# Performance work log

Measured on AMD Instinct MI355X. Metric: run time of the kernel, lower is better.

## Reference

```python
import jax, jax.numpy as jnp
import numpy as np

H = 16      # num_attention_heads
HKV = 4     # num_key_value_heads
HIDDEN = 1024
HEAD_DIM = HIDDEN // H  # 64
ROPE_BASE = 10000.0


def _rope(x):
    # Rotate-half RoPE applied over the FULL projected last dim, matching the
    # module which applies self._rope before splitting into heads.
    B, S, D = x.shape
    half = D // 2
    inv_freq = 1.0 / (ROPE_BASE ** (jnp.arange(half, dtype=jnp.float32) / half))
    ang = jnp.arange(S, dtype=jnp.float32)[:, None] * inv_freq[None, :]  # [S, half]
    cos, sin = jnp.cos(ang), jnp.sin(ang)
    x1, x2 = x[..., :half], x[..., half:]
    return jnp.concatenate([x1 * cos - x2 * sin, x2 * cos + x1 * sin], axis=-1)


def _rmsnorm(x):
    # F.rms_norm with no weight: x / sqrt(mean(x^2) + eps)
    eps = jnp.finfo(x.dtype).eps
    return x * jax.lax.rsqrt(jnp.mean(x * x, axis=-1, keepdims=True) + eps)


def setup_inputs() -> dict:
    key = jax.random.key(0)
    ks = jax.random.split(key, 10)
    B, S = 2, 2048
    kv_dim = HKV * HEAD_DIM
    sc = 0.02
    return {
        "hidden_state": jax.random.normal(ks[0], (B, S, HIDDEN), dtype=jnp.float32),
        "attention_mask": jnp.zeros((B, S, S), dtype=jnp.float32),
        "Wq": jax.random.normal(ks[1], (HIDDEN, HIDDEN), dtype=jnp.float32) * sc,
        "bq": jnp.zeros((HIDDEN,), dtype=jnp.float32),
        "Wk": jax.random.normal(ks[2], (HIDDEN, kv_dim), dtype=jnp.float32) * sc,
        "bk": jnp.zeros((kv_dim,), dtype=jnp.float32),
        "Wv": jax.random.normal(ks[3], (HIDDEN, kv_dim), dtype=jnp.float32) * sc,
        "bv": jnp.zeros((kv_dim,), dtype=jnp.float32),
        "Wo": jax.random.normal(ks[4], (HIDDEN, HIDDEN), dtype=jnp.float32) * sc,
        "bo": jnp.zeros((HIDDEN,), dtype=jnp.float32),
    }


def reference(hidden_state, attention_mask, Wq, bq, Wk, bk, Wv, bv, Wo, bo):
    B, S, _ = hidden_state.shape
    G = H // HKV  # query heads per kv head
    d = HEAD_DIM

    q = hidden_state @ Wq + bq            # [B,S,H*d]
    k = hidden_state @ Wk + bk            # [B,S,Hkv*d]
    v = hidden_state @ Wv + bv            # [B,S,Hkv*d]

    q = _rope(q)
    k = _rope(k)

    # split heads; repeat_interleave of KV over groups == grouping Q heads as [Hkv, G]
    q = q.reshape(B, S, H, d).transpose(0, 2, 1, 3).reshape(B, HKV, G, S, d)
    k = k.reshape(B, S, HKV, d).transpose(0, 2, 1, 3)   # [B,Hkv,S,d]
    v = v.reshape(B, S, HKV, d).transpose(0, 2, 1, 3)   # [B,Hkv,S,d]

    q = _rmsnorm(q)
    k = _rmsnorm(k)

    scale = d ** 0.5
    scores = jnp.einsum('bkgqd,bksd->bkgqs', q, k) / scale  # [B,Hkv,G,S,S]
    scores = scores + attention_mask[:, None, None, :, :]
    attn = jax.nn.softmax(scores, axis=-1)
    out = jnp.einsum('bkgqs,bksd->bkgqd', attn, v)          # [B,Hkv,G,S,d]

    out = out.reshape(B, H, S, d).transpose(0, 2, 1, 3).reshape(B, S, H * d)
    return out @ Wo + bo
```

## Files before the change

kernel.cpp:

```cpp
#include <hip/hip_runtime.h>
#include <cmath>

#define SEQ 2048
#define BATCH 2
#define HID 1024
#define NH 16
#define NKV 4
#define DH 64
#define KVDIM 256
#define K32C 32

typedef __attribute__((ext_vector_type(8))) short bf16x8;
typedef __attribute__((ext_vector_type(4))) float f32x4;

static __device__ __forceinline__ unsigned short f2bf(float x) {
  union { float f; unsigned u; } v; v.f = x;
  unsigned r = v.u + 0x7fffu + ((v.u >> 16) & 1u);
  return (unsigned short)(r >> 16);
}
static __device__ __forceinline__ float bf2f(unsigned short h) {
  union { unsigned u; float f; } v; v.u = ((unsigned)h) << 16;
  return v.f;
}
static __device__ __forceinline__ void gl_lds16(const void* g, void* l) {
  __builtin_amdgcn_global_load_lds(
      (const __attribute__((address_space(1))) unsigned int*)g,
      (__attribute__((address_space(3))) unsigned int*)l, 16, 0, 0);
}

template<bool HILO>
__global__ __launch_bounds__(256) void pack_a_kernel(
    const float* __restrict__ A, unsigned short* __restrict__ hi,
    unsigned short* __restrict__ lo) {
  int gid = blockIdx.x * 256 + threadIdx.x;
  int lane = gid & 63;
  int k32 = (gid >> 6) & 31;
  int m16 = gid >> 11;
  int quad = lane >> 4, l16 = lane & 15;
  const float* src = A + (size_t)(m16 * 16 + l16) * 1024 + k32 * 32 + quad * 8;
  float4 a0 = *(const float4*)src;
  float4 a1 = *(const float4*)(src + 4);
  float v[8] = {a0.x, a0.y, a0.z, a0.w, a1.x, a1.y, a1.z, a1.w};
  unsigned short h[8], l[8];
#pragma unroll
  for (int j = 0; j < 8; ++j) {
    h[j] = f2bf(v[j]);
    if (HILO) l[j] = f2bf(v[j] - bf2f(h[j]));
  }
  *(bf16x8*)(hi + (size_t)gid * 8) = *(bf16x8*)h;
  if (HILO) *(bf16x8*)(lo + (size_t)gid * 8) = *(bf16x8*)l;
}

__global__ __launch_bounds__(256) void pack_a_norm_kernel(
    const float* __restrict__ A, const float* __restrict__ lpart,
    unsigned short* __restrict__ hi, unsigned short* __restrict__ lo) {
  int gid = blockIdx.x * 256 + threadIdx.x;
  int lane = gid & 63;
  int k32 = (gid >> 6) & 31;
  int m16 = gid >> 11;
  int quad = lane >> 4, l16 = lane & 15;
  int m = m16 * 16 + l16;
  int b = m >> 11, s = m & 2047;
  int k0 = k32 * 32 + quad * 8;
  int h = k0 >> 6;
  float inv = 1.0f / lpart[(size_t)(b * NH + h) * SEQ + s];
  const float* src = A + (size_t)m * 1024 + k0;
  float4 a0 = *(const float4*)src;
  float4 a1 = *(const float4*)(src + 4);
  float v[8] = {a0.x, a0.y, a0.z, a0.w, a1.x, a1.y, a1.z, a1.w};
  unsigned short hh[8], ll[8];
#pragma unroll
  for (int j = 0; j < 8; ++j) {
    float x = v[j] * inv;
    hh[j] = f2bf(x);
    ll[j] = f2bf(x - bf2f(hh[j]));
  }
  *(bf16x8*)(hi + (size_t)gid * 8) = *(bf16x8*)hh;
  *(bf16x8*)(lo + (size_t)gid * 8) = *(bf16x8*)ll;
}

template<bool HILO>
__global__ __launch_bounds__(256) void pack_b_kernel(
    const float* __restrict__ W, unsigned short* __restrict__ hi,
    unsigned short* __restrict__ lo, int Nsrc) {
  int gid = blockIdx.x * 256 + threadIdx.x;
  int lane = gid & 63;
  int k32 = (gid >> 6) & 31;
  int n16 = gid >> 11;
  int quad = lane >> 4, l16 = lane & 15;
  int n = n16 * 16 + l16, k = k32 * 32 + quad * 8;
  unsigned short h[8], l[8];
#pragma unroll
  for (int j = 0; j < 8; ++j) {
    float v = W[(size_t)(k + j) * Nsrc + n];
    h[j] = f2bf(v);
    if (HILO) l[j] = f2bf(v - bf2f(h[j]));
  }
  *(bf16x8*)(hi + (size_t)gid * 8) = *(bf16x8*)h;
  if (HILO) *(bf16x8*)(lo + (size_t)gid * 8) = *(bf16x8*)l;
}

__global__ __launch_bounds__(256) void bias_cat_kernel(
    const float* __restrict__ bq, const float* __restrict__ bk,
    const float* __restrict__ bv, float* __restrict__ dst) {
  int n = blockIdx.x * 256 + threadIdx.x;
  if (n < 1536)
    dst[n] = (n < 1024) ? bq[n] : (n < 1280 ? bk[n - 1024] : bv[n - 1280]);
}

template<int CHAINS, bool OUTBF16>
__global__ __launch_bounds__(256) void gemm_pk_kernel(
    const unsigned short* __restrict__ Ah, const unsigned short* __restrict__ Al,
    const unsigned short* __restrict__ Bh, const unsigned short* __restrict__ Bl,
    const float* __restrict__ bias, void* __restrict__ Cout, int N) {
  constexpr int NCH = (CHAINS == 3) ? 2 : 1;
  __shared__ unsigned short Asm[NCH][4 * 512];
  __shared__ unsigned short Bsm[NCH][8 * 512];
  const int tid = threadIdx.x;
  const int wave = tid >> 6, lane = tid & 63;
  const int wr = wave >> 1, wc = wave & 1;
  const int quad = lane >> 4, l16 = lane & 15;
  const size_t abase = ((size_t)(blockIdx.y * 4 + wave) * K32C) * 64 + lane;
  const size_t bbase0 = ((size_t)(blockIdx.x * 8 + wave) * K32C) * 64 + lane;
  const size_t bbase1 = ((size_t)(blockIdx.x * 8 + wave + 4) * K32C) * 64 + lane;
  f32x4 acc[2][4] = {};
  for (int k32 = 0; k32 < K32C; ++k32) {
    __syncthreads();
    gl_lds16(Ah + (abase + (size_t)k32 * 64) * 8, &Asm[0][wave * 512]);
    gl_lds16(Bh + (bbase0 + (size_t)k32 * 64) * 8, &Bsm[0][wave * 512]);
    gl_lds16(Bh + (bbase1 + (size_t)k32 * 64) * 8, &Bsm[0][(wave + 4) * 512]);
    if (CHAINS == 3) {
      gl_lds16(Al + (abase + (size_t)k32 * 64) * 8, &Asm[1][wave * 512]);
      gl_lds16(Bl + (bbase0 + (size_t)k32 * 64) * 8, &Bsm[1][wave * 512]);
      gl_lds16(Bl + (bbase1 + (size_t)k32 * 64) * 8, &Bsm[1][(wave + 4) * 512]);
    }
    __syncthreads();
    bf16x8 af[2][NCH], bfr[4][NCH];
#pragma unroll
    for (int mt = 0; mt < 2; ++mt)
#pragma unroll
      for (int ch = 0; ch < NCH; ++ch)
        af[mt][ch] = *(const bf16x8*)&Asm[ch][((wr * 2 + mt) * 64 + lane) * 8];
#pragma unroll
    for (int nt = 0; nt < 4; ++nt)
#pragma unroll
      for (int ch = 0; ch < NCH; ++ch)
        bfr[nt][ch] = *(const bf16x8*)&Bsm[ch][((wc * 4 + nt) * 64 + lane) * 8];
#pragma unroll
    for (int mt = 0; mt < 2; ++mt)
#pragma unroll
      for (int nt = 0; nt < 4; ++nt) {
        acc[mt][nt] = __builtin_amdgcn_mfma_f32_16x16x32_bf16(af[mt][0], bfr[nt][0], acc[mt][nt], 0, 0, 0);
        if (CHAINS == 3) {
          acc[mt][nt] = __builtin_amdgcn_mfma_f32_16x16x32_bf16(af[mt][1], bfr[nt][0], acc[mt][nt], 0, 0, 0);
          acc[mt][nt] = __builtin_amdgcn_mfma_f32_16x16x32_bf16(af[mt][0], bfr[nt][1], acc[mt][nt], 0, 0, 0);
        }
      }
  }
  const int n0 = blockIdx.x * 128 + wc * 64;
  const int m0 = blockIdx.y * 64 + wr * 32;
#pragma unroll
  for (int mt = 0; mt < 2; ++mt)
#pragma unroll
    for (int nt = 0; nt < 4; ++nt)
#pragma unroll
      for (int r = 0; r < 4; ++r) {
        int gm = m0 + mt * 16 + quad * 4 + r;
        int n = n0 + nt * 16 + l16;
        float v = acc[mt][nt][r] + bias[n];
        if (OUTBF16)
          ((unsigned short*)Cout)[(size_t)gm * N + n] = f2bf(v);
        else
          ((float*)Cout)[(size_t)gm * N + n] = v;
      }
}

__global__ __launch_bounds__(1024) void rope_norm_q_kernel(
    const unsigned short* __restrict__ qkv, unsigned short* __restrict__ Qh,
    unsigned short* __restrict__ Ql) {
  const int s = blockIdx.x, b = blockIdx.y;
  const int t = threadIdx.x;
  const unsigned short* row = qkv + ((size_t)b * SEQ + s) * 1536;
  const int j = t & 511;
  float invf = exp2f((float)j * (-13.287712379549449f / 512.0f));
  float ang = (float)s * invf;
  float c = cosf(ang), sn = sinf(ang);
  float x1 = bf2f(row[j]), x2 = bf2f(row[j + 512]);
  float val = (t < 512) ? (x1 * c - x2 * sn) : (x2 * c + x1 * sn);
  float ss = val * val;
#pragma unroll
  for (int off = 1; off < 64; off <<= 1) ss += __shfl_xor(ss, off);
  float rn = rsqrtf(ss * (1.0f / 64.0f) + 1.1920929e-07f);
  float v = val * rn;
  unsigned short hi = f2bf(v);
  unsigned short lo = f2bf(v - bf2f(hi));
  int h = t >> 6, d = t & 63;
  size_t o = (size_t)(b * NH + h) * 131072 +
             ((((size_t)(s >> 4) * 2 + (d >> 5)) * 64) + ((d >> 3) & 3) * 16 + (s & 15)) * 8 + (d & 7);
  Qh[o] = hi;
  Ql[o] = lo;
}

__global__ __launch_bounds__(256) void rope_norm_kv_kernel(
    const unsigned short* __restrict__ qkv, unsigned short* __restrict__ Kpk,
    unsigned short* __restrict__ Vpk) {
  const int s = blockIdx.x, b = blockIdx.y;
  const int t = threadIdx.x;
  const unsigned short* row = qkv + ((size_t)b * SEQ + s) * 1536;
  const int j = t & 127;
  float invf = exp2f((float)j * (-13.287712379549449f / 128.0f));
  float ang = (float)s * invf;
  float c = cosf(ang), sn = sinf(ang);
  float x1 = bf2f(row[1024 + j]), x2 = bf2f(row[1024 + 128 + j]);
  float val = (t < 128) ? (x1 * c - x2 * sn) : (x2 * c + x1 * sn);
  float ss = val * val;
#pragma unroll
  for (int off = 1; off < 64; off <<= 1) ss += __shfl_xor(ss, off);
  float rn = rsqrtf(ss * (1.0f / 64.0f) + 1.1920929e-07f);
  float kv = val * rn;
  int h = t >> 6, d = t & 63;
  size_t ko = (size_t)(b * NKV + h) * 131072 +
              ((((size_t)(s >> 4) * 2 + (d >> 5)) * 64) + ((d >> 3) & 3) * 16 + (s & 15)) * 8 + (d & 7);
  Kpk[ko] = f2bf(kv);
  size_t vo = (size_t)(b * NKV + h) * 131072 +
              ((((size_t)(d >> 4) * 64 + (s >> 5)) * 64) + ((s >> 3) & 3) * 16 + (d & 15)) * 8 + (s & 7);
  Vpk[vo] = row[1280 + t];
}

__global__ __launch_bounds__(256, 4) void attn_mfma5_kernel(
    const unsigned short* __restrict__ Qh, const unsigned short* __restrict__ Ql,
    const unsigned short* __restrict__ Kpk, const unsigned short* __restrict__ Vpk,
    const float* __restrict__ mask, float* __restrict__ attn_po,
    float* __restrict__ l_part) {
  __shared__ __align__(16) unsigned short Kb[2][4 * 512];
  __shared__ __align__(16) unsigned short Vb[2][4 * 512];
  __shared__ __align__(16) float Msk[2][32 * 32];
  __shared__ __align__(16) unsigned short Ps[4][16 * 72];

  const int b = blockIdx.z;
  const int kvh = blockIdx.y >> 1, jh = blockIdx.y & 1;
  const int q0 = blockIdx.x * 32;
  const int tid = threadIdx.x, wave = tid >> 6, lane = tid & 63;
  const int quad = lane >> 4, l16 = lane & 15;
  const int h = kvh * 4 + wave;

  bf16x8 qh[2][2], ql[2][2];
  {
    const unsigned short* Qb_h = Qh + (size_t)(b * NH + h) * 131072;
    const unsigned short* Qb_l = Ql + (size_t)(b * NH + h) * 131072;
#pragma unroll
    for (int mt = 0; mt < 2; ++mt)
#pragma unroll
      for (int kf = 0; kf < 2; ++kf) {
        size_t o = ((((size_t)(q0 >> 4) + mt) * 2 + kf) * 64 + lane) * 8;
        qh[mt][kf] = *(const bf16x8*)(Qb_h + o);
        ql[mt][kf] = *(const bf16x8*)(Qb_l + o);
      }
  }

  const unsigned short* Kbase = Kpk + (size_t)(b * NKV + kvh) * 131072;
  const unsigned short* Vbase = Vpk + (size_t)(b * NKV + kvh) * 131072;
  const int jbase = jh * (SEQ / 2);

  const float* mbase = mask + ((size_t)b * SEQ + q0) * SEQ + jbase;
  const int srow = wave * 8 + (lane >> 3);
  const int ssw = ((srow >> 2) & 1) << 4;
  const float* msrc0 = mbase + (size_t)srow * SEQ + (((lane & 7) * 4) ^ ssw);

  bf16x8 ones;
#pragma unroll
  for (int i = 0; i < 8; ++i) ones[i] = (short)0x3F80;

  f32x4 O[2][4] = {};
  f32x4 lAcc[2] = {};

  auto stage = [&](int buf, int jc) {
    const int j0 = jbase + jc * 32;
    gl_lds16(Kbase + ((((size_t)(j0 >> 4) + (wave >> 1)) * 2 + (wave & 1)) * 64 + lane) * 8,
             &Kb[buf][wave * 512]);
    gl_lds16(Vbase + (((size_t)wave * 64 + (j0 >> 5)) * 64 + lane) * 8,
             &Vb[buf][wave * 512]);
    gl_lds16(msrc0 + jc * 32, &Msk[buf][wave * 256]);
  };

  stage(0, 0);
  for (int jc = 0; jc < 32; ++jc) {
    const int cur = jc & 1;
    __syncthreads();
    if (jc < 31) stage(cur ^ 1, jc + 1);

    bf16x8 kbf[2][2], vbf[4];
#pragma unroll
    for (int nt = 0; nt < 2; ++nt)
#pragma unroll
      for (int kf = 0; kf < 2; ++kf)
        kbf[nt][kf] = *(const bf16x8*)&Kb[cur][((nt * 2 + kf) * 64 + lane) * 8];
#pragma unroll
    for (int d16 = 0; d16 < 4; ++d16)
      vbf[d16] = *(const bf16x8*)&Vb[cur][(d16 * 64 + lane) * 8];

    bf16x8 pa[2];
#pragma unroll
    for (int mt = 0; mt < 2; ++mt) {
#pragma unroll
      for (int nt = 0; nt < 2; ++nt) {
        f32x4 C = {};
        C = __builtin_amdgcn_mfma_f32_16x16x32_bf16(qh[mt][0], kbf[nt][0], C, 0, 0, 0);
        C = __builtin_amdgcn_mfma_f32_16x16x32_bf16(qh[mt][1], kbf[nt][1], C, 0, 0, 0);
        C = __builtin_amdgcn_mfma_f32_16x16x32_bf16(ql[mt][0], kbf[nt][0], C, 0, 0, 0);
        C = __builtin_amdgcn_mfma_f32_16x16x32_bf16(ql[mt][1], kbf[nt][1], C, 0, 0, 0);
#pragma unroll
        for (int r = 0; r < 4; ++r) {
          int row16 = quad * 4 + r;
          float m = Msk[cur][(mt * 16 + row16) * 32 +
                             ((nt * 16 + l16) ^ ((quad & 1) << 4))];
          float p = exp2f(fmaf(C[r], 0.18033688f,
                               fmaf(m, 1.44269504f, -11.54156033f)));
          union { float f; unsigned u; } pu; pu.f = p;
          Ps[wave][row16 * 72 + nt * 16 + l16] = (unsigned short)((pu.u + 0x8000u) >> 16);
        }
      }
      pa[mt] = *(const bf16x8*)&Ps[wave][l16 * 72 + quad * 8];
    }
#pragma unroll
    for (int mt = 0; mt < 2; ++mt) {
      lAcc[mt] = __builtin_amdgcn_mfma_f32_16x16x32_bf16(pa[mt], ones, lAcc[mt], 0, 0, 0);
#pragma unroll
      for (int nt = 0; nt < 4; ++nt)
        O[mt][nt] = __builtin_amdgcn_mfma_f32_16x16x32_bf16(pa[mt], vbf[nt], O[mt][nt], 0, 0, 0);
    }
  }

#pragma unroll
  for (int mt = 0; mt < 2; ++mt)
#pragma unroll
    for (int r = 0; r < 4; ++r) {
      int s = q0 + mt * 16 + quad * 4 + r;
#pragma unroll
      for (int nt = 0; nt < 4; ++nt)
        atomicAdd(attn_po + ((size_t)b * SEQ + s) * HID + h * DH + nt * 16 + l16,
                  O[mt][nt][r]);
      if (l16 == 0)
        atomicAdd(l_part + (size_t)(b * NH + h) * SEQ + s, lAcc[mt][r]);
    }
}

extern "C" void kernel_launch(void* const* d_in, const int* in_sizes, int n_in,
                              void* d_out, int out_size, void* d_ws, size_t ws_size,
                              hipStream_t stream) {
  const float* hs   = (const float*)d_in[0];
  const float* mask = (const float*)d_in[1];
  const float* Wq   = (const float*)d_in[2];
  const float* bq   = (const float*)d_in[3];
  const float* Wk   = (const float*)d_in[4];
  const float* bk   = (const float*)d_in[5];
  const float* Wv   = (const float*)d_in[6];
  const float* bv   = (const float*)d_in[7];
  const float* Wo   = (const float*)d_in[8];
  const float* bo   = (const float*)d_in[9];
  float* out = (float*)d_out;
  char* ws = (char*)d_ws;
  const size_t MiB = 1048576;

  unsigned short* hs_pk   = (unsigned short*)(ws);
  unsigned short* qkvproj = (unsigned short*)(ws + 8 * MiB);
  float*          attn_po = (float*)(ws);
  float*          l_part  = (float*)(ws + 16 * MiB);
  unsigned short* Wqkv_hi = (unsigned short*)(ws + 20 * MiB);
  unsigned short* Wo_hi   = (unsigned short*)(ws + 20 * MiB);
  unsigned short* Wo_lo   = (unsigned short*)(ws + 22 * MiB);
  unsigned short* Qpk_h   = (unsigned short*)(ws + 24 * MiB);
  unsigned short* Qpk_l   = (unsigned short*)(ws + 32 * MiB);
  unsigned short* ao_hi   = (unsigned short*)(ws + 24 * MiB);
  unsigned short* ao_lo   = (unsigned short*)(ws + 32 * MiB);
  unsigned short* Kpk     = (unsigned short*)(ws + 40 * MiB);
  unsigned short* Vpk     = (unsigned short*)(ws + 42 * MiB);
  float*          bias_c  = (float*)(ws + 44 * MiB);

  pack_a_kernel<false><<<2048, 256, 0, stream>>>(hs, hs_pk, nullptr);
  pack_b_kernel<false><<<512, 256, 0, stream>>>(Wq, Wqkv_hi, nullptr, 1024);
  pack_b_kernel<false><<<128, 256, 0, stream>>>(Wk, Wqkv_hi + (size_t)64 * 2048 * 8, nullptr, 256);
  pack_b_kernel<false><<<128, 256, 0, stream>>>(Wv, Wqkv_hi + (size_t)80 * 2048 * 8, nullptr, 256);
  bias_cat_kernel<<<6, 256, 0, stream>>>(bq, bk, bv, bias_c);

  gemm_pk_kernel<1, true><<<dim3(12, 64), 256, 0, stream>>>(
      hs_pk, nullptr, Wqkv_hi, nullptr, bias_c, qkvproj, 1536);

  pack_b_kernel<true><<<512, 256, 0, stream>>>(Wo, Wo_hi, Wo_lo, 1024);

  rope_norm_q_kernel<<<dim3(SEQ, BATCH), dim3(1024), 0, stream>>>(qkvproj, Qpk_h, Qpk_l);
  rope_norm_kv_kernel<<<dim3(SEQ, BATCH), dim3(256), 0, stream>>>(qkvproj, Kpk, Vpk);

  hipMemsetAsync(ws, 0, 16 * MiB + 262144, stream);
  attn_mfma5_kernel<<<dim3(SEQ / 32, NKV * 2, BATCH), 256, 0, stream>>>(
      Qpk_h, Qpk_l, Kpk, Vpk, mask, attn_po, l_part);

  pack_a_norm_kernel<<<2048, 256, 0, stream>>>(attn_po, l_part, ao_hi, ao_lo);
  gemm_pk_kernel<3, false><<<dim3(8, 64), 256, 0, stream>>>(
      ao_hi, ao_lo, Wo_hi, Wo_lo, bo, out, 1024);
}
```

Measured before the change: 298.2 us.

## Merge split-KV attention halves in-block via LDS instead of global atomics

The two KV-halves of attention now run as two groups of four waves in one 512-thread block and combine their partial outputs and row sums through shared memory. The normalization by the row sum moves into the attention epilogue. This removes the workspace memset, the global float atomics and the separate normalizing pack kernel. It also swaps exp2f for the hardware exp2 builtin. The cost is 66KB of LDS per block and an extra barrier, which may lower occupancy.

After: 270.6 us. 1.1x faster.

```diff
diff --git a/kernel.cpp b/kernel.cpp
--- a/kernel.cpp
+++ b/kernel.cpp
@@ -49,34 +49,6 @@
   }
   *(bf16x8*)(hi + (size_t)gid * 8) = *(bf16x8*)h;
   if (HILO) *(bf16x8*)(lo + (size_t)gid * 8) = *(bf16x8*)l;
-}
-
-__global__ __launch_bounds__(256) void pack_a_norm_kernel(
-    const float* __restrict__ A, const float* __restrict__ lpart,
-    unsigned short* __restrict__ hi, unsigned short* __restrict__ lo) {
-  int gid = blockIdx.x * 256 + threadIdx.x;
-  int lane = gid & 63;
-  int k32 = (gid >> 6) & 31;
-  int m16 = gid >> 11;
-  int quad = lane >> 4, l16 = lane & 15;
-  int m = m16 * 16 + l16;
-  int b = m >> 11, s = m & 2047;
-  int k0 = k32 * 32 + quad * 8;
-  int h = k0 >> 6;
-  float inv = 1.0f / lpart[(size_t)(b * NH + h) * SEQ + s];
-  const float* src = A + (size_t)m * 1024 + k0;
-  float4 a0 = *(const float4*)src;
-  float4 a1 = *(const float4*)(src + 4);
-  float v[8] = {a0.x, a0.y, a0.z, a0.w, a1.x, a1.y, a1.z, a1.w};
-  unsigned short hh[8], ll[8];
-#pragma unroll
-  for (int j = 0; j < 8; ++j) {
-    float x = v[j] * inv;
-    hh[j] = f2bf(x);
-    ll[j] = f2bf(x - bf2f(hh[j]));
-  }
-  *(bf16x8*)(hi + (size_t)gid * 8) = *(bf16x8*)hh;
-  *(bf16x8*)(lo + (size_t)gid * 8) = *(bf16x8*)ll;
 }
 
 template<bool HILO>
@@ -227,22 +199,22 @@
   Vpk[vo] = row[1280 + t];
 }
 
-__global__ __launch_bounds__(256, 4) void attn_mfma5_kernel(
+__global__ __launch_bounds__(512, 4) void attn_mfma6_kernel(
     const unsigned short* __restrict__ Qh, const unsigned short* __restrict__ Ql,
     const unsigned short* __restrict__ Kpk, const unsigned short* __restrict__ Vpk,
-    const float* __restrict__ mask, float* __restrict__ attn_po,
-    float* __restrict__ l_part) {
-  __shared__ __align__(16) unsigned short Kb[2][4 * 512];
-  __shared__ __align__(16) unsigned short Vb[2][4 * 512];
-  __shared__ __align__(16) float Msk[2][32 * 32];
-  __shared__ __align__(16) unsigned short Ps[4][16 * 72];
-
-  const int b = blockIdx.z;
-  const int kvh = blockIdx.y >> 1, jh = blockIdx.y & 1;
+    const float* __restrict__ mask, float* __restrict__ attn_o) {
+  __shared__ __align__(16) char smem[67584];
+  unsigned short* Kb = (unsigned short*)smem;
+  unsigned short* Vb = (unsigned short*)(smem + 16384);
+  float*          Msk = (float*)(smem + 32768);
+  unsigned short* Ps = (unsigned short*)(smem + 49152);
+
+  const int b = blockIdx.z, kvh = blockIdx.y;
   const int q0 = blockIdx.x * 32;
   const int tid = threadIdx.x, wave = tid >> 6, lane = tid & 63;
+  const int jh = wave >> 2, w4 = wave & 3;
   const int quad = lane >> 4, l16 = lane & 15;
-  const int h = kvh * 4 + wave;
+  const int h = kvh * 4 + w4;
 
   bf16x8 qh[2][2], ql[2][2];
   {
@@ -260,10 +232,9 @@
 
   const unsigned short* Kbase = Kpk + (size_t)(b * NKV + kvh) * 131072;
   const unsigned short* Vbase = Vpk + (size_t)(b * NKV + kvh) * 131072;
-  const int jbase = jh * (SEQ / 2);
-
-  const float* mbase = mask + ((size_t)b * SEQ + q0) * SEQ + jbase;
-  const int srow = wave * 8 + (lane >> 3);
+
+  const float* mbase = mask + ((size_t)b * SEQ + q0) * SEQ;
+  const int srow = w4 * 8 + (lane >> 3);
   const int ssw = ((srow >> 2) & 1) << 4;
   const float* msrc0 = mbase + (size_t)srow * SEQ + (((lane & 7) * 4) ^ ssw);
 
@@ -275,12 +246,12 @@
   f32x4 lAcc[2] = {};
 
   auto stage = [&](int buf, int jc) {
-    const int j0 = jbase + jc * 32;
-    gl_lds16(Kbase + ((((size_t)(j0 >> 4) + (wave >> 1)) * 2 + (wave & 1)) * 64 + lane) * 8,
-             &Kb[buf][wave * 512]);
-    gl_lds16(Vbase + (((size_t)wave * 64 + (j0 >> 5)) * 64 + lane) * 8,
-             &Vb[buf][wave * 512]);
-    gl_lds16(msrc0 + jc * 32, &Msk[buf][wave * 256]);
+    const int j0 = jh * (SEQ / 2) + jc * 32;
+    gl_lds16(Kbase + ((((size_t)(j0 >> 4) + (w4 >> 1)) * 2 + (w4 & 1)) * 64 + lane) * 8,
+             Kb + (buf * 2 + jh) * 2048 + w4 * 512);
+    gl_lds16(Vbase + (((size_t)w4 * 64 + (j0 >> 5)) * 64 + lane) * 8,
+             Vb + (buf * 2 + jh) * 2048 + w4 * 512);
+    gl_lds16(msrc0 + j0, Msk + (buf * 2 + jh) * 1024 + w4 * 256);
   };
 
   stage(0, 0);
@@ -294,10 +265,10 @@
     for (int nt = 0; nt < 2; ++nt)
 #pragma unroll
       for (int kf = 0; kf < 2; ++kf)
-        kbf[nt][kf] = *(const bf16x8*)&Kb[cur][((nt * 2 + kf) * 64 + lane) * 8];
+        kbf[nt][kf] = *(const bf16x8*)&Kb[(cur * 2 + jh) * 2048 + ((nt * 2 + kf) * 64 + lane) * 8];
 #pragma unroll
     for (int d16 = 0; d16 < 4; ++d16)
-      vbf[d16] = *(const bf16x8*)&Vb[cur][(d16 * 64 + lane) * 8];
+      vbf[d16] = *(const bf16x8*)&Vb[(cur * 2 + jh) * 2048 + (d16 * 64 + lane) * 8];
 
     bf16x8 pa[2];
 #pragma unroll
@@ -312,15 +283,16 @@
 #pragma unroll
         for (int r = 0; r < 4; ++r) {
           int row16 = quad * 4 + r;
-          float m = Msk[cur][(mt * 16 + row16) * 32 +
-                             ((nt * 16 + l16) ^ ((quad & 1) << 4))];
-          float p = exp2f(fmaf(C[r], 0.18033688f,
-                               fmaf(m, 1.44269504f, -11.54156033f)));
+          float m = Msk[(cur * 2 + jh) * 1024 + (mt * 16 + row16) * 32 +
+                        ((nt * 16 + l16) ^ ((quad & 1) << 4))];
+          float p = __builtin_amdgcn_exp2f(
+              fmaf(C[r], 0.18033688f, fmaf(m, 1.44269504f, -11.54156033f)));
           union { float f; unsigned u; } pu; pu.f = p;
-          Ps[wave][row16 * 72 + nt * 16 + l16] = (unsigned short)((pu.u + 0x8000u) >> 16);
+          Ps[wave * 1152 + row16 * 72 + nt * 16 + l16] =
+              (unsigned short)((pu.u + 0x8000u) >> 16);
         }
       }
-      pa[mt] = *(const bf16x8*)&Ps[wave][l16 * 72 + quad * 8];
+      pa[mt] = *(const bf16x8*)&Ps[wave * 1152 + l16 * 72 + quad * 8];
     }
 #pragma unroll
     for (int mt = 0; mt < 2; ++mt) {
@@ -331,18 +303,37 @@
     }
   }
 
-#pragma unroll
-  for (int mt = 0; mt < 2; ++mt)
-#pragma unroll
-    for (int r = 0; r < 4; ++r) {
-      int s = q0 + mt * 16 + quad * 4 + r;
-#pragma unroll
-      for (int nt = 0; nt < 4; ++nt)
-        atomicAdd(attn_po + ((size_t)b * SEQ + s) * HID + h * DH + nt * 16 + l16,
-                  O[mt][nt][r]);
-      if (l16 == 0)
-        atomicAdd(l_part + (size_t)(b * NH + h) * SEQ + s, lAcc[mt][r]);
-    }
+  __syncthreads();
+  float* Oex = (float*)smem;
+  float* lex = (float*)(smem + 34816);
+  if (jh == 1) {
+#pragma unroll
+    for (int mt = 0; mt < 2; ++mt)
+#pragma unroll
+      for (int r = 0; r < 4; ++r) {
+        int row = mt * 16 + quad * 4 + r;
+#pragma unroll
+        for (int nt = 0; nt < 4; ++nt)
+          Oex[((size_t)w4 * 32 + row) * 68 + nt * 16 + l16] = O[mt][nt][r];
+        if (l16 == 0) lex[w4 * 32 + row] = lAcc[mt][r];
+      }
+  }
+  __syncthreads();
+  if (jh == 0) {
+    float* po = attn_o + ((size_t)b * SEQ + q0) * HID + h * DH;
+#pragma unroll
+    for (int mt = 0; mt < 2; ++mt)
+#pragma unroll
+      for (int r = 0; r < 4; ++r) {
+        int row = mt * 16 + quad * 4 + r;
+        float inv = 1.0f / (lAcc[mt][r] + lex[w4 * 32 + row]);
+#pragma unroll
+        for (int nt = 0; nt < 4; ++nt) {
+          float v = (O[mt][nt][r] + Oex[((size_t)w4 * 32 + row) * 68 + nt * 16 + l16]) * inv;
+          po[(size_t)row * HID + nt * 16 + l16] = v;
+        }
+      }
+  }
 }
 
 extern "C" void kernel_launch(void* const* d_in, const int* in_sizes, int n_in,
@@ -364,8 +355,7 @@
 
   unsigned short* hs_pk   = (unsigned short*)(ws);
   unsigned short* qkvproj = (unsigned short*)(ws + 8 * MiB);
-  float*          attn_po = (float*)(ws);
-  float*          l_part  = (float*)(ws + 16 * MiB);
+  float*          attn_o  = (float*)(ws);
   unsigned short* Wqkv_hi = (unsigned short*)(ws + 20 * MiB);
   unsigned short* Wo_hi   = (unsigned short*)(ws + 20 * MiB);
   unsigned short* Wo_lo   = (unsigned short*)(ws + 22 * MiB);
@@ -391,11 +381,10 @@
   rope_norm_q_kernel<<<dim3(SEQ, BATCH), dim3(1024), 0, stream>>>(qkvproj, Qpk_h, Qpk_l);
   rope_norm_kv_kernel<<<dim3(SEQ, BATCH), dim3(256), 0, stream>>>(qkvproj, Kpk, Vpk);
 
-  hipMemsetAsync(ws, 0, 16 * MiB + 262144, stream);
-  attn_mfma5_kernel<<<dim3(SEQ / 32, NKV * 2, BATCH), 256, 0, stream>>>(
-      Qpk_h, Qpk_l, Kpk, Vpk, mask, attn_po, l_part);
-
-  pack_a_norm_kernel<<<2048, 256, 0, stream>>>(attn_po, l_part, ao_hi, ao_lo);
+  attn_mfma6_kernel<<<dim3(SEQ / 32, NKV, BATCH), dim3(512), 0, stream>>>(
+      Qpk_h, Qpk_l, Kpk, Vpk, mask, attn_o);
+
+  pack_a_kernel<true><<<2048, 256, 0, stream>>>(attn_o, ao_hi, ao_lo);
   gemm_pk_kernel<3, false><<<dim3(8, 64), 256, 0, stream>>>(
       ao_hi, ao_lo, Wo_hi, Wo_lo, bo, out, 1024);
 }
```
